# Kernel optimization log

Hardware: AMD Instinct MI355X
Metric: run time of the kernel (lower is better)

Reference implementation:

```python
import jax, jax.numpy as jnp
import numpy as np

N = [40000, 10000, 2500, 625, 157]  # vertex counts per mesh level (0 = full res)
K = 6


def _propagate(x, row, col, norm, n):
    # x: [B, N_in, C]; gather neighbor feats, weight by norm, scatter-add to rows
    msg = x[:, col, :] * norm[None, :, None]          # [B, E, C]
    return jnp.zeros((x.shape[0], n, x.shape[2]), x.dtype).at[:, row, :].add(msg)


def cheb_conv(x, edge_index, W, b, n):
    # Chebyshev graph conv with sym-normalized adjacency (lambda_max=2 / CoMA convention)
    row, col = edge_index[0], edge_index[1]
    deg = jnp.zeros((n,), x.dtype).at[row].add(jnp.ones(row.shape, x.dtype))
    dinv = jnp.where(deg > 0, deg ** -0.5, jnp.zeros_like(deg))
    norm = dinv[row] * dinv[col]
    Tx0 = x
    out = jnp.einsum('bnc,cd->bnd', Tx0, W[0])
    Tx1 = _propagate(Tx0, row, col, norm, n)
    out = out + jnp.einsum('bnc,cd->bnd', Tx1, W[1])
    for k in range(2, W.shape[0]):
        Tx2 = 2.0 * _propagate(Tx1, row, col, norm, n) - Tx0
        out = out + jnp.einsum('bnc,cd->bnd', Tx2, W[k])
        Tx0, Tx1 = Tx1, Tx2
    return out + b


def pool(x, row, col, val, n_out):
    # sparse COO upsampling: out[:, row] += val * x[:, col]  (Pool() in torch source)
    msg = x[:, col, :] * val[None, :, None]
    return jnp.zeros((x.shape[0], n_out, x.shape[2]), x.dtype).at[:, row, :].add(msg)


def setup_inputs() -> dict:
    key = jax.random.key(0)
    ks = iter(jax.random.split(key, 64))
    B, latent = 16, 128
    inp = {}
    inp['x'] = jax.random.normal(next(ks), (B, latent), jnp.float32)
    inp['lin_w'] = jax.random.normal(next(ks), (latent, N[4] * 64), jnp.float32) * 0.05
    inp['lin_b'] = jnp.zeros((N[4] * 64,), jnp.float32)
    for i in range(4):
        inp[f'edge{i}'] = jax.random.randint(next(ks), (2, 6 * N[i]), 0, N[i])
    for i in range(4):
        nnz = 3 * N[i]
        inp[f'up{i}_row'] = jax.random.randint(next(ks), (nnz,), 0, N[i])
        inp[f'up{i}_col'] = jax.random.randint(next(ks), (nnz,), 0, N[i + 1])
        inp[f'up{i}_val'] = jax.random.uniform(next(ks), (nnz,), jnp.float32)
    # Deblock Cheb weights: (in,out) = (64,64),(64,32),(32,32),(32,32); final (32,3)
    for j, (ci, co) in enumerate([(64, 64), (64, 32), (32, 32), (32, 32)], start=1):
        inp[f'W{j}'] = jax.random.normal(next(ks), (K, ci, co), jnp.float32) * 0.05
        inp[f'b{j}'] = jnp.zeros((co,), jnp.float32)
    inp['Wout'] = jax.random.normal(next(ks), (K, 32, 3), jnp.float32) * 0.05
    inp['bout'] = jnp.zeros((3,), jnp.float32)
    return inp


def reference(x, lin_w, lin_b, edge0, edge1, edge2, edge3,
              up0_row, up0_col, up0_val, up1_row, up1_col, up1_val,
              up2_row, up2_col, up2_val, up3_row, up3_col, up3_val,
              W1, b1, W2, b2, W3, b3, W4, b4, Wout, bout):
    B = x.shape[0]
    h = (x @ lin_w + lin_b).reshape(B, N[4], 64)        # latent -> coarsest mesh
    edges = [edge0, edge1, edge2, edge3]
    ups = [(up0_row, up0_col, up0_val), (up1_row, up1_col, up1_val),
           (up2_row, up2_col, up2_val), (up3_row, up3_col, up3_val)]
    Ws = [(W1, b1), (W2, b2), (W3, b3), (W4, b4)]
    for j in range(4):
        lvl = 3 - j  # deblock j upsamples to mesh level lvl (coarse -> fine)
        row, col, val = ups[lvl]
        h = pool(h, row, col, val, N[lvl])
        h = jax.nn.elu(cheb_conv(h, edges[lvl], Ws[j][0], Ws[j][1], N[lvl]))
    return cheb_conv(h, edge0, Wout, bout, N[0])        # [B, 40000, 3]
```

## Files before the change

### kernel.cpp

```cpp
#include <hip/hip_runtime.h>
#include <math.h>

#define TB 256
#define SCAN_TOT 106250
#define SCAN_NB  104

typedef __bf16 bf16x8 __attribute__((ext_vector_type(8)));
typedef float f32x4 __attribute__((ext_vector_type(4)));
typedef float f32x2 __attribute__((ext_vector_type(2)));

static __device__ __forceinline__ int gtid() { return blockIdx.x * blockDim.x + threadIdx.x; }

static __device__ __forceinline__ void fma4(float4& a, float s, const float4 b) {
  a.x = fmaf(s, b.x, a.x); a.y = fmaf(s, b.y, a.y);
  a.z = fmaf(s, b.z, a.z); a.w = fmaf(s, b.w, a.w);
}

static __device__ __forceinline__ float bfus(unsigned short u) {
  union { unsigned u; float f; } c; c.u = ((unsigned)u) << 16; return c.f;
}
static __device__ __forceinline__ unsigned pk2(float a, float b) {
  union { unsigned u; __bf16 h[2]; } c;
  c.h[0] = (__bf16)a; c.h[1] = (__bf16)b;
  return c.u;
}
static __device__ __forceinline__ unsigned short us1(float a) {
  union { unsigned short u; __bf16 h; } c; c.h = (__bf16)a; return c.u;
}
static __device__ __forceinline__ f32x2 unpk(unsigned u) {
  union { unsigned u; float f; } lo, hi;
  lo.u = u << 16; hi.u = u & 0xffff0000u;
  f32x2 r; r.x = lo.f; r.y = hi.f; return r;
}

__global__ void fill_kernel(float* __restrict__ p, int n, float v) {
  int i = gtid(); if (i < n) p[i] = v;
}

__global__ void zero_int_kernel(int* __restrict__ p, int n) {
  int i = gtid(); if (i < n) p[i] = 0;
}

struct SegD {
  const int* rows[8];
  const int* cols[8];
  const float* vals[8];
  int start[8];
  int degb[8];
};

__global__ void count_all_kernel(SegD sg, int total, int* __restrict__ deg) {
  int t = gtid(); if (t >= total) return;
  int seg = 0;
  #pragma unroll
  for (int q = 1; q < 8; ++q) seg += (t >= sg.start[q]);
  int i = t - sg.start[seg];
  atomicAdd(&deg[sg.degb[seg] + sg.rows[seg][i]], 1);
}

__global__ void fill_all_kernel(SegD sg, int total, const int* __restrict__ deg,
                                const int* __restrict__ offs, int* __restrict__ cursor,
                                int2* __restrict__ cwc) {
  int t = gtid(); if (t >= total) return;
  int seg = 0;
  #pragma unroll
  for (int q = 1; q < 8; ++q) seg += (t >= sg.start[q]);
  int i = t - sg.start[seg];
  int db = sg.degb[seg];
  int r = sg.rows[seg][i];
  int c = sg.cols[seg][i];
  int p = atomicAdd(&cursor[db + r], 1);
  int idx = offs[db + r] + p;
  float w;
  if (sg.vals[seg]) {
    w = sg.vals[seg][i];
  } else {
    int dc = deg[db + c];
    w = rsqrtf((float)deg[db + r]) * (dc > 0 ? rsqrtf((float)dc) : 0.f);
  }
  int2 o; o.x = c; o.y = __float_as_int(w);
  cwc[idx] = o;
}

__global__ void scan_phase1(const int* __restrict__ in, int* __restrict__ bsum) {
  __shared__ int wsum[4];
  int blk = blockIdx.x, t = threadIdx.x;
  int base = blk * 1024 + t * 4;
  int s = 0;
  #pragma unroll
  for (int q = 0; q < 4; ++q) { int i = base + q; if (i < SCAN_TOT) s += in[i]; }
  #pragma unroll
  for (int o = 32; o > 0; o >>= 1) s += __shfl_xor(s, o, 64);
  int lane = t & 63, wid = t >> 6;
  if (lane == 0) wsum[wid] = s;
  __syncthreads();
  if (t == 0) bsum[blk] = wsum[0] + wsum[1] + wsum[2] + wsum[3];
}

__global__ void scan_phase2(int* __restrict__ bsum, int* __restrict__ offs_end) {
  int t = threadIdx.x;
  int v = (t < SCAN_NB) ? bsum[t] : 0;
  int lane = t & 63, wid = t >> 6;
  int p = v;
  #pragma unroll
  for (int o = 1; o < 64; o <<= 1) { int u = __shfl_up(p, o, 64); if (lane >= o) p += u; }
  __shared__ int w0tot;
  if (wid == 0 && lane == 63) w0tot = p;
  __syncthreads();
  int incl = p + (wid ? w0tot : 0);
  if (t < SCAN_NB) bsum[t] = incl - v;
  if (t == 127) offs_end[0] = incl;
}

__global__ void scan_phase3(const int* __restrict__ in, const int* __restrict__ bbase,
                            int* __restrict__ offs, int* __restrict__ cursor) {
  __shared__ int wsum[4];
  int blk = blockIdx.x, t = threadIdx.x;
  int base = blk * 1024 + t * 4;
  int v[4]; int s = 0;
  #pragma unroll
  for (int q = 0; q < 4; ++q) { int i = base + q; v[q] = (i < SCAN_TOT) ? in[i] : 0; s += v[q]; }
  int lane = t & 63, wid = t >> 6;
  int p = s;
  #pragma unroll
  for (int o = 1; o < 64; o <<= 1) { int u = __shfl_up(p, o, 64); if (lane >= o) p += u; }
  if (lane == 63) wsum[wid] = p;
  __syncthreads();
  int woff = 0;
  #pragma unroll
  for (int q = 0; q < 4; ++q) woff += (q < wid) ? wsum[q] : 0;
  int ex = bbase[blk] + woff + p - s;
  #pragma unroll
  for (int q = 0; q < 4; ++q) {
    int i = base + q;
    if (i < SCAN_TOT) { offs[i] = ex; cursor[i] = 0; ex += v[q]; }
  }
}

__global__ void wconv_kernel(const float* __restrict__ W, unsigned* __restrict__ Wt) {
  int p = gtid();
  if (p >= 6 * 32 * 16) return;
  int kk2 = p & 15;
  int col = (p >> 4) & 31;
  int kidx = p >> 9;
  float v0 = W[kidx * 1024 + (2 * kk2) * 32 + col];
  float v1 = W[kidx * 1024 + (2 * kk2 + 1) * 32 + col];
  Wt[(kidx * 32 + col) * 16 + kk2] = pk2(v0, v1);
}

__global__ void pool_kernel(const float4* __restrict__ x, const int* __restrict__ offs,
                            const int2* __restrict__ cwc,
                            float4* __restrict__ out, int n, int xs4, int xoff4,
                            int os4, int osh) {
  int t = gtid();
  if (t >= n * os4) return;
  int v = t >> osh, j = t & (os4 - 1);
  int s = offs[v], e = offs[v + 1];
  float4 a = {0.f, 0.f, 0.f, 0.f};
  for (int i = s; i < e; ++i) {
    int2 cw = cwc[i];
    fma4(a, __int_as_float(cw.y), x[(long long)cw.x * xs4 + xoff4 + j]);
  }
  out[t] = a;
}

template<int SRC>
__global__ void __launch_bounds__(256)
pool_mfma_kernel(const void* __restrict__ xsrc, const int* __restrict__ offs,
                 const int2* __restrict__ cwc,
                 uint4* __restrict__ Xout, uint4* __restrict__ b5out,
                 const uint4* __restrict__ Wtk5, int n) {
  int lane = threadIdx.x & 63;
  int v = (blockIdx.x << 2) | (threadIdx.x >> 6);
  if (v >= n) return;
  int g = lane >> 4, c15 = lane & 15;
  int s = offs[v], e = offs[v + 1];
  int deg = e - s;
  float a[8];
  #pragma unroll
  for (int q = 0; q < 8; ++q) a[q] = 0.f;

  if (deg > 0) {
    if (SRC == 0) {
      const float4* x = (const float4*)xsrc;
      float4 x0[4], x1[4]; float ww[4];
      #pragma unroll
      for (int p = 0; p < 4; ++p) {
        int idx = s + (p < deg ? p : 0);
        int2 cw = cwc[idx];
        ww[p] = (p < deg) ? __int_as_float(cw.y) : 0.f;
        const float4* xr = x + (long long)cw.x * 128 + c15 * 8 + g * 2;
        x0[p] = xr[0]; x1[p] = xr[1];
      }
      #pragma unroll
      for (int p = 0; p < 4; ++p) {
        float w = ww[p];
        a[0] = fmaf(w, x0[p].x, a[0]); a[1] = fmaf(w, x0[p].y, a[1]);
        a[2] = fmaf(w, x0[p].z, a[2]); a[3] = fmaf(w, x0[p].w, a[3]);
        a[4] = fmaf(w, x1[p].x, a[4]); a[5] = fmaf(w, x1[p].y, a[5]);
        a[6] = fmaf(w, x1[p].z, a[6]); a[7] = fmaf(w, x1[p].w, a[7]);
      }
      for (int i = s + 4; i < e; ++i) {
        int2 cw = cwc[i];
        float w = __int_as_float(cw.y);
        const float4* xr = x + (long long)cw.x * 128 + c15 * 8 + g * 2;
        float4 y0 = xr[0], y1 = xr[1];
        a[0] = fmaf(w, y0.x, a[0]); a[1] = fmaf(w, y0.y, a[1]);
        a[2] = fmaf(w, y0.z, a[2]); a[3] = fmaf(w, y0.w, a[3]);
        a[4] = fmaf(w, y1.x, a[4]); a[5] = fmaf(w, y1.y, a[5]);
        a[6] = fmaf(w, y1.z, a[6]); a[7] = fmaf(w, y1.w, a[7]);
      }
    } else {
      const uint4* x = (const uint4*)xsrc;
      uint4 bv[4]; float ww[4];
      #pragma unroll
      for (int p = 0; p < 4; ++p) {
        int idx = s + (p < deg ? p : 0);
        int2 cw = cwc[idx];
        ww[p] = (p < deg) ? __int_as_float(cw.y) : 0.f;
        bv[p] = x[(long long)cw.x * 64 + c15 * 4 + g];
      }
      #pragma unroll
      for (int p = 0; p < 4; ++p) {
        f32x2 w2 = {ww[p], ww[p]};
        f32x2 r0 = __builtin_elementwise_fma(w2, unpk(bv[p].x), f32x2{a[0], a[1]});
        f32x2 r1 = __builtin_elementwise_fma(w2, unpk(bv[p].y), f32x2{a[2], a[3]});
        f32x2 r2 = __builtin_elementwise_fma(w2, unpk(bv[p].z), f32x2{a[4], a[5]});
        f32x2 r3 = __builtin_elementwise_fma(w2, unpk(bv[p].w), f32x2{a[6], a[7]});
        a[0] = r0.x; a[1] = r0.y; a[2] = r1.x; a[3] = r1.y;
        a[4] = r2.x; a[5] = r2.y; a[6] = r3.x; a[7] = r3.y;
      }
      for (int i = s + 4; i < e; ++i) {
        int2 cw = cwc[i];
        float w = __int_as_float(cw.y);
        f32x2 w2 = {w, w};
        uint4 xv = x[(long long)cw.x * 64 + c15 * 4 + g];
        f32x2 r0 = __builtin_elementwise_fma(w2, unpk(xv.x), f32x2{a[0], a[1]});
        f32x2 r1 = __builtin_elementwise_fma(w2, unpk(xv.y), f32x2{a[2], a[3]});
        f32x2 r2 = __builtin_elementwise_fma(w2, unpk(xv.z), f32x2{a[4], a[5]});
        f32x2 r3 = __builtin_elementwise_fma(w2, unpk(xv.w), f32x2{a[6], a[7]});
        a[0] = r0.x; a[1] = r0.y; a[2] = r1.x; a[3] = r1.y;
        a[4] = r2.x; a[5] = r2.y; a[6] = r3.x; a[7] = r3.y;
      }
    }
  }
  union { uint4 u; bf16x8 b; } Au;
  Au.u.x = pk2(a[0], a[1]); Au.u.y = pk2(a[2], a[3]);
  Au.u.z = pk2(a[4], a[5]); Au.u.w = pk2(a[6], a[7]);
  Xout[(long long)v * 64 + c15 * 4 + g] = Au.u;

  union { uint4 u; bf16x8 b; } B0u, B1u;
  B0u.u = Wtk5[c15 * 4 + g];
  B1u.u = Wtk5[(16 + c15) * 4 + g];
  f32x4 z = {0.f, 0.f, 0.f, 0.f};
  f32x4 m0 = __builtin_amdgcn_mfma_f32_16x16x32_bf16(Au.b, B0u.b, z, 0, 0, 0);
  f32x4 m1 = __builtin_amdgcn_mfma_f32_16x16x32_bf16(Au.b, B1u.b, z, 0, 0, 0);
  uint4 o;
  o.x = pk2(m0[0], m1[0]); o.y = pk2(m0[1], m1[1]);
  o.z = pk2(m0[2], m1[2]); o.w = pk2(m0[3], m1[3]);
  b5out[(long long)v * 64 + g * 16 + c15] = o;
}

template<int CIN, int COUT>
__global__ void cheb_step_kernel(const float* __restrict__ X,
                                 const float* __restrict__ b1,
                                 float* __restrict__ b2o,
                                 const float* __restrict__ Wk,
                                 const float* __restrict__ bias,
                                 const int* __restrict__ offs,
                                 const int2* __restrict__ cwc,
                                 int n, int LB, int mode) {
  constexpr int CS = COUT / 8;
  constexpr int LCS = (CS == 8) ? 3 : 2;
  constexpr int W4 = COUT / 4;
  __shared__ float sW[CIN * COUT];
  for (int i = threadIdx.x; i < CIN * COUT; i += blockDim.x) sW[i] = Wk[i];
  __syncthreads();
  int t = gtid();
  int BI = 1 << LB;
  if (t >= n * BI * CS) return;
  int cs = t & (CS - 1);
  int r = t >> LCS;
  int v = r >> LB;
  int bi = r & (BI - 1);
  float4 a0 = {0.f, 0.f, 0.f, 0.f}, a1 = {0.f, 0.f, 0.f, 0.f};
  const float4* Xr = (const float4*)(X + (long long)r * CIN);
  const float4* wbase = ((const float4*)sW) + cs * 2;
  #pragma unroll
  for (int c4 = 0; c4 < CIN / 4; ++c4) {
    float4 xv = Xr[c4];
    const float4* w = wbase + (c4 * 4) * W4;
    fma4(a0, xv.x, w[0]); fma4(a1, xv.x, w[1]); w += W4;
    fma4(a0, xv.y, w[0]); fma4(a1, xv.y, w[1]); w += W4;
    fma4(a0, xv.z, w[0]); fma4(a1, xv.z, w[1]); w += W4;
    fma4(a0, xv.w, w[0]); fma4(a1, xv.w, w[1]);
  }
  if (mode >= 1) {
    float sc = (mode == 3) ? 1.f : 2.f;
    int s = offs[v], e = offs[v + 1];
    const float4* b14 = (const float4*)b1;
    for (int i = s; i < e; ++i) {
      int2 cw = cwc[i];
      float w = __int_as_float(cw.y) * sc;
      long long rb = (long long)((cw.x << LB) | bi) * W4 + cs * 2;
      fma4(a0, w, b14[rb]); fma4(a1, w, b14[rb + 1]);
    }
  }
  float4* Or = ((float4*)b2o) + (long long)r * W4 + cs * 2;
  if (mode >= 2) {
    float4 p0 = Or[0], p1 = Or[1];
    a0.x -= p0.x; a0.y -= p0.y; a0.z -= p0.z; a0.w -= p0.w;
    a1.x -= p1.x; a1.y -= p1.y; a1.z -= p1.z; a1.w -= p1.w;
  }
  if (mode == 3) {
    const float* bs = bias + cs * 8;
    a0.x += bs[0]; a0.y += bs[1]; a0.z += bs[2]; a0.w += bs[3];
    a1.x += bs[4]; a1.y += bs[5]; a1.z += bs[6]; a1.w += bs[7];
    a0.x = a0.x > 0.f ? a0.x : expm1f(a0.x);
    a0.y = a0.y > 0.f ? a0.y : expm1f(a0.y);
    a0.z = a0.z > 0.f ? a0.z : expm1f(a0.z);
    a0.w = a0.w > 0.f ? a0.w : expm1f(a0.w);
    a1.x = a1.x > 0.f ? a1.x : expm1f(a1.x);
    a1.y = a1.y > 0.f ? a1.y : expm1f(a1.y);
    a1.z = a1.z > 0.f ? a1.z : expm1f(a1.z);
    a1.w = a1.w > 0.f ? a1.w : expm1f(a1.w);
  }
  Or[0] = a0; Or[1] = a1;
}

__global__ void __launch_bounds__(256)
cheb_mfma32_kernel(const uint4* __restrict__ X,
                   const uint4* __restrict__ b1,
                   uint4* __restrict__ b2o,
                   const uint4* __restrict__ Wtk,
                   const float* __restrict__ bias,
                   const int* __restrict__ offs,
                   const int2* __restrict__ cwc,
                   int n, int mode) {
  int lane = threadIdx.x & 63;
  int v = (blockIdx.x << 2) | (threadIdx.x >> 6);
  if (v >= n) return;
  int g = lane >> 4;
  int c15 = lane & 15;

  union { uint4 u; bf16x8 b; } Au, B0u, B1u;
  Au.u = X[(long long)v * 64 + c15 * 4 + g];
  B0u.u = Wtk[c15 * 4 + g];
  B1u.u = Wtk[(16 + c15) * 4 + g];

  f32x4 z = {0.f, 0.f, 0.f, 0.f};
  f32x4 m0 = __builtin_amdgcn_mfma_f32_16x16x32_bf16(Au.b, B0u.b, z, 0, 0, 0);
  f32x4 m1 = __builtin_amdgcn_mfma_f32_16x16x32_bf16(Au.b, B1u.b, z, 0, 0, 0);
  f32x2 acc[4];
  #pragma unroll
  for (int q = 0; q < 4; ++q) { acc[q].x = m0[q]; acc[q].y = m1[q]; }

  long long own = (long long)v * 64 + g * 16 + c15;
  if (mode >= 1) {
    float sc = (mode == 3) ? 1.f : 2.f;
    int s = offs[v], e = offs[v + 1];
    int deg = e - s;
    if (deg > 0) {
      uint4 bv[8]; float ww[8];
      #pragma unroll
      for (int p = 0; p < 8; ++p) {
        int idx = s + (p < deg ? p : 0);
        int2 cw = cwc[idx];
        ww[p] = (p < deg) ? __int_as_float(cw.y) * sc : 0.f;
        bv[p] = b1[(long long)cw.x * 64 + g * 16 + c15];
      }
      #pragma unroll
      for (int p = 0; p < 8; ++p) {
        f32x2 w2 = {ww[p], ww[p]};
        acc[0] = __builtin_elementwise_fma(w2, unpk(bv[p].x), acc[0]);
        acc[1] = __builtin_elementwise_fma(w2, unpk(bv[p].y), acc[1]);
        acc[2] = __builtin_elementwise_fma(w2, unpk(bv[p].z), acc[2]);
        acc[3] = __builtin_elementwise_fma(w2, unpk(bv[p].w), acc[3]);
      }
      for (int i = s + 8; i < e; ++i) {
        int2 cw = cwc[i];
        float w = __int_as_float(cw.y) * sc;
        f32x2 w2 = {w, w};
        uint4 xv = b1[(long long)cw.x * 64 + g * 16 + c15];
        acc[0] = __builtin_elementwise_fma(w2, unpk(xv.x), acc[0]);
        acc[1] = __builtin_elementwise_fma(w2, unpk(xv.y), acc[1]);
        acc[2] = __builtin_elementwise_fma(w2, unpk(xv.z), acc[2]);
        acc[3] = __builtin_elementwise_fma(w2, unpk(xv.w), acc[3]);
      }
    }
  }
  if (mode >= 2) {
    uint4 pv = b2o[own];
    acc[0] -= unpk(pv.x); acc[1] -= unpk(pv.y);
    acc[2] -= unpk(pv.z); acc[3] -= unpk(pv.w);
  }
  if (mode == 3) {
    float bs0 = bias[c15], bs1 = bias[16 + c15];
    unsigned short* o = (unsigned short*)b2o;
    long long lb = ((long long)v * 16 + 4 * g) * 32;
    #pragma unroll
    for (int q = 0; q < 4; ++q) {
      float a = acc[q].x + bs0;
      float b = acc[q].y + bs1;
      a = a > 0.f ? a : expm1f(a);
      b = b > 0.f ? b : expm1f(b);
      o[lb + q * 32 + c15] = us1(a);
      o[lb + q * 32 + 16 + c15] = us1(b);
    }
  } else {
    uint4 o;
    o.x = pk2(acc[0].x, acc[0].y); o.y = pk2(acc[1].x, acc[1].y);
    o.z = pk2(acc[2].x, acc[2].y); o.w = pk2(acc[3].x, acc[3].y);
    b2o[own] = o;
  }
}

__global__ void gemm_out_all_kernel(const uint4* __restrict__ X, const float* __restrict__ W,
                                    unsigned short* __restrict__ c_all, int nr) {
  __shared__ float sW[576];
  for (int i = threadIdx.x; i < 576; i += blockDim.x) sW[i] = W[i];
  __syncthreads();
  int r = gtid();
  if (r >= nr) return;
  const uint4* Xr = X + (long long)r * 4;
  float xa[32];
  #pragma unroll
  for (int q = 0; q < 4; ++q) {
    uint4 xv = Xr[q];
    f32x2 p0 = unpk(xv.x), p1 = unpk(xv.y), p2 = unpk(xv.z), p3 = unpk(xv.w);
    xa[q * 8 + 0] = p0.x; xa[q * 8 + 1] = p0.y;
    xa[q * 8 + 2] = p1.x; xa[q * 8 + 3] = p1.y;
    xa[q * 8 + 4] = p2.x; xa[q * 8 + 5] = p2.y;
    xa[q * 8 + 6] = p3.x; xa[q * 8 + 7] = p3.y;
  }
  float acc[18];
  #pragma unroll
  for (int i = 0; i < 18; ++i) acc[i] = 0.f;
  #pragma unroll
  for (int c = 0; c < 32; ++c) {
    float xc = xa[c];
    #pragma unroll
    for (int k = 0; k < 6; ++k) {
      acc[k * 3 + 0] = fmaf(xc, sW[k * 96 + c * 3 + 0], acc[k * 3 + 0]);
      acc[k * 3 + 1] = fmaf(xc, sW[k * 96 + c * 3 + 1], acc[k * 3 + 1]);
      acc[k * 3 + 2] = fmaf(xc, sW[k * 96 + c * 3 + 2], acc[k * 3 + 2]);
    }
  }
  #pragma unroll
  for (int k = 0; k < 6; ++k) {
    unsigned short* o = c_all + ((long long)k * nr + r) * 3;
    o[0] = us1(acc[k * 3 + 0]);
    o[1] = us1(acc[k * 3 + 1]);
    o[2] = us1(acc[k * 3 + 2]);
  }
}

__global__ void cheb_out_step_kernel(const unsigned short* __restrict__ c_all, int k,
                                     const float* __restrict__ b1,
                                     float* __restrict__ b2o,
                                     const float* __restrict__ bias,
                                     const int* __restrict__ offs,
                                     const int2* __restrict__ cwc,
                                     int n, float* __restrict__ dout, int mode) {
  int r = gtid();
  if (r >= n * 16) return;
  int v = r >> 4, bi = r & 15;
  const unsigned short* cr = c_all + ((long long)k * n * 16 + r) * 3;
  float a0 = bfus(cr[0]), a1 = bfus(cr[1]), a2 = bfus(cr[2]);
  if (mode >= 1) {
    float sc = (mode == 3) ? 1.f : 2.f;
    int s = offs[v], e = offs[v + 1];
    for (int i = s; i < e; ++i) {
      int2 cw = cwc[i];
      float w = __int_as_float(cw.y) * sc;
      const float* br = b1 + (long long)((cw.x << 4) | bi) * 3;
      a0 = fmaf(w, br[0], a0); a1 = fmaf(w, br[1], a1); a2 = fmaf(w, br[2], a2);
    }
  }
  if (mode >= 2) {
    const float* p = b2o + (long long)r * 3;
    a0 -= p[0]; a1 -= p[1]; a2 -= p[2];
  }
  if (mode == 3) {
    a0 += bias[0]; a1 += bias[1]; a2 += bias[2];
    float* o = dout + ((long long)bi * n + v) * 3;
    o[0] = a0; o[1] = a1; o[2] = a2;
  } else {
    float* o = b2o + (long long)r * 3;
    o[0] = a0; o[1] = a1; o[2] = a2;
  }
}

__global__ void linear_kernel(const float* __restrict__ x, const float* __restrict__ w,
                              const float* __restrict__ bias, float* __restrict__ out) {
  int t = gtid();
  const int TOT = 157 * 16 * 64;
  if (t >= TOT) return;
  int c = t & 63;
  int b = (t >> 6) & 15;
  int v = t >> 10;
  int colw = v * 64 + c;
  float acc = bias[colw];
  const float* xr = x + b * 128;
  for (int k = 0; k < 128; ++k) acc = fmaf(xr[k], w[k * 10048 + colw], acc);
  out[t] = acc;
}

extern "C" void kernel_launch(void* const* d_in, const int* in_sizes, int n_in,
                              void* d_out, int out_size, void* d_ws, size_t ws_size,
                              hipStream_t stream) {
  const int N[4] = {40000, 10000, 2500, 625};
  const int E[4] = {240000, 60000, 15000, 3750};
  const int NNZ[4] = {120000, 30000, 7500, 1875};
  const int DP[4] = {0, 40000, 50000, 52500};
  const int DE[4] = {53125, 93125, 103125, 105625};
  const int ITEMS = 478125;

  const float* x     = (const float*)d_in[0];
  const float* lin_w = (const float*)d_in[1];
  const float* lin_b = (const float*)d_in[2];
  const int* edge[4] = {(const int*)d_in[3], (const int*)d_in[4], (const int*)d_in[5], (const int*)d_in[6]};
  const int* up_row[4]; const int* up_col[4]; const float* up_val[4];
  for (int i = 0; i < 4; ++i) {
    up_row[i] = (const int*)d_in[7 + 3 * i];
    up_col[i] = (const int*)d_in[8 + 3 * i];
    up_val[i] = (const float*)d_in[9 + 3 * i];
  }
  const float* W_[5] = {(const float*)d_in[19], (const float*)d_in[21], (const float*)d_in[23],
                        (const float*)d_in[25], (const float*)d_in[27]};
  const float* b_[5] = {(const float*)d_in[20], (const float*)d_in[22], (const float*)d_in[24],
                        (const float*)d_in[26], (const float*)d_in[28]};

  char* ws = (char*)d_ws;
  size_t off = 0;
  auto alloc = [&](size_t bytes) -> void* {
    void* p = ws + off;
    off = (off + bytes + 255) & ~(size_t)255;
    return p;
  };
  auto cdiv = [](int a, int b) { return (a + b - 1) / b; };

  float* slot[4];
  for (int i = 0; i < 4; ++i) slot[i] = (float*)alloc(20480000ull);
  uint4* Ab = (uint4*)alloc(40960000ull);
  uint4* Bb = (uint4*)alloc(40960000ull);
  uint4* Cb = (uint4*)alloc(40960000ull);
  unsigned short* c_all = (unsigned short*)alloc((size_t)6 * 640000 * 3 * 2);
  float* ob1 = (float*)alloc((size_t)640000 * 3 * 4);
  float* ob2 = (float*)alloc((size_t)640000 * 3 * 4);
  int* deg_all    = (int*)alloc(SCAN_TOT * 4);
  int* cursor_all = (int*)alloc(SCAN_TOT * 4);
  int* offs_all   = (int*)alloc((SCAN_TOT + 1) * 4);
  int* bsum       = (int*)alloc(SCAN_NB * 4);
  int2* cwc_arena = (int2*)alloc((size_t)ITEMS * 8);
  uint4* Wt2 = (uint4*)alloc(6 * 128 * 16);
  uint4* Wt3 = (uint4*)alloc(6 * 128 * 16);

  if (off > ws_size) {
    fill_kernel<<<cdiv(out_size, TB), TB, 0, stream>>>((float*)d_out, out_size,
                                                       (float)(ws_size >> 20));
    return;
  }

  SegD sg;
  int cum = 0;
  for (int l = 0; l < 4; ++l) {
    sg.rows[l] = up_row[l]; sg.cols[l] = up_col[l]; sg.vals[l] = up_val[l];
    sg.start[l] = cum; sg.degb[l] = DP[l]; cum += NNZ[l];
  }
  for (int l = 0; l < 4; ++l) {
    sg.rows[4 + l] = edge[l]; sg.cols[4 + l] = edge[l] + E[l]; sg.vals[4 + l] = nullptr;
    sg.start[4 + l] = cum; sg.degb[4 + l] = DE[l]; cum += E[l];
  }
  zero_int_kernel<<<cdiv(SCAN_TOT, TB), TB, 0, stream>>>(deg_all, SCAN_TOT);
  count_all_kernel<<<cdiv(ITEMS, TB), TB, 0, stream>>>(sg, ITEMS, deg_all);
  scan_phase1<<<SCAN_NB, TB, 0, stream>>>(deg_all, bsum);
  scan_phase2<<<1, 128, 0, stream>>>(bsum, offs_all + SCAN_TOT);
  scan_phase3<<<SCAN_NB, TB, 0, stream>>>(deg_all, bsum, offs_all, cursor_all);
  fill_all_kernel<<<cdiv(ITEMS, TB), TB, 0, stream>>>(sg, ITEMS, deg_all, offs_all,
                                                      cursor_all, cwc_arena);
  wconv_kernel<<<cdiv(3072, TB), TB, 0, stream>>>(W_[2], (unsigned*)Wt2);
  wconv_kernel<<<cdiv(3072, TB), TB, 0, stream>>>(W_[3], (unsigned*)Wt3);

  linear_kernel<<<cdiv(157 * 16 * 64, TB), TB, 0, stream>>>(x, lin_w, lin_b, slot[0]);
  float* H = slot[0];
  float* A = slot[1];
  float* B = slot[2];
  float* C = slot[3];

  const int CINA[2]  = {64, 64};
  const int COUTA[2] = {64, 32};

  for (int j = 0; j < 2; ++j) {
    int lvl = 3 - j;
    int n = N[lvl];
    int cin = CINA[j], cout = COUTA[j];
    int os4 = 16 * cin / 4;
    int osh = (os4 == 256) ? 8 : 7;
    const int* offs_p = offs_all + DP[lvl];
    const int* offs_e = offs_all + DE[lvl];

    pool_kernel<<<cdiv(n * os4, TB), TB, 0, stream>>>(
        (const float4*)H, offs_p, cwc_arena, (float4*)A, n, os4, 0, os4, osh);

    int cs = cout / 8;
    dim3 g(cdiv(n * 16 * cs, TB));
    auto step = [&](const float* b1, float* b2o, int k, int mode) {
      const float* Wk = W_[j] + (size_t)k * cin * cout;
      if (cin == 64 && cout == 64)
        hipLaunchKernelGGL((cheb_step_kernel<64, 64>), g, dim3(TB), 0, stream,
                           A, b1, b2o, Wk, b_[j], offs_e, cwc_arena, n, 4, mode);
      else
        hipLaunchKernelGGL((cheb_step_kernel<64, 32>), g, dim3(TB), 0, stream,
                           A, b1, b2o, Wk, b_[j], offs_e, cwc_arena, n, 4, mode);
    };
    step(nullptr, B, 5, 0);
    step(B, C, 4, 1);
    step(C, B, 3, 2);
    step(B, C, 2, 2);
    step(C, B, 1, 2);
    step(B, C, 0, 3);

    float* tmp = H; H = C; C = tmp;
  }
  float* freeA = A;
  float* freeB = B;
  float* freeC = C;

  uint4* Ab1 = (uint4*)freeA;
  uint4* Bb1 = (uint4*)freeB;
  uint4* Cb1 = (uint4*)freeC;
  {
    int n = N[1];
    dim3 gmf(n / 4);
    hipLaunchKernelGGL((pool_mfma_kernel<0>), gmf, dim3(256), 0, stream,
                       (const void*)H, offs_all + DP[1], cwc_arena,
                       Ab1, Bb1, Wt2 + (size_t)5 * 128, n);
    auto dstep = [&](const uint4* b1, uint4* b2o, int k, int mode) {
      cheb_mfma32_kernel<<<gmf, dim3(256), 0, stream>>>(
          Ab1, b1, b2o, Wt2 + (size_t)k * 128, b_[2],
          offs_all + DE[1], cwc_arena, n, mode);
    };
    dstep(Bb1, Cb1, 4, 1);
    dstep(Cb1, Bb1, 3, 2);
    dstep(Bb1, Cb1, 2, 2);
    dstep(Cb1, Bb1, 1, 2);
    dstep(Bb1, Cb1, 0, 3);
  }

  {
    int n = N[0];
    int nr = n * 16;
    const int* offs_e = offs_all + DE[0];
    dim3 gmf(n / 4);

    hipLaunchKernelGGL((pool_mfma_kernel<1>), gmf, dim3(256), 0, stream,
                       (const void*)Cb1, offs_all + DP[0], cwc_arena,
                       Ab, Bb, Wt3 + (size_t)5 * 128, n);

    auto dstep = [&](const uint4* b1, uint4* b2o, int k, int mode) {
      cheb_mfma32_kernel<<<gmf, dim3(256), 0, stream>>>(
          Ab, b1, b2o, Wt3 + (size_t)k * 128, b_[3],
          offs_e, cwc_arena, n, mode);
    };
    dstep(Bb, Cb, 4, 1);
    dstep(Cb, Bb, 3, 2);
    dstep(Bb, Cb, 2, 2);
    dstep(Cb, Bb, 1, 2);
    dstep(Bb, Cb, 0, 3);

    dim3 gr(cdiv(nr, TB));
    gemm_out_all_kernel<<<gr, dim3(TB), 0, stream>>>((const uint4*)Cb, W_[4], c_all, nr);
    float* dout = (float*)d_out;
    auto ostep = [&](const float* b1, float* b2o, int k, int mode) {
      cheb_out_step_kernel<<<gr, dim3(TB), 0, stream>>>(
          c_all, k, b1, b2o, b_[4], offs_e, cwc_arena, n, dout, mode);
    };
    ostep(nullptr, ob1, 5, 0);
    ostep(ob1, ob2, 4, 1);
    ostep(ob2, ob1, 3, 2);
    ostep(ob1, ob2, 2, 2);
    ostep(ob2, ob1, 1, 2);
    ostep(ob1, ob2, 0, 3);
  }
}
```

Baseline: 748.9 us.

## Split finest-level decoder into two batch halves to shrink working buffers

Processes the level-0 pool, Chebyshev steps and output conv in two passes of 8 batch samples each. The pool and cheb MFMA kernels are templated on rows-per-vertex R so that one 16-row MFMA tile covers two vertices when R is 8. Intermediate buffers are halved, so each pass's working set is smaller and more of it may stay in the MI355X's large last-level cache. The trade-off is twice as many kernel launches, re-reading the edge lists per pass, and more complex index mapping.

```diff
diff --git a/kernel.cpp b/kernel.cpp
--- a/kernel.cpp
+++ b/kernel.cpp
@@ -164,17 +164,22 @@
   out[t] = a;
 }
 
-template<int SRC>
+template<int SRC, int R>
 __global__ void __launch_bounds__(256)
 pool_mfma_kernel(const void* __restrict__ xsrc, const int* __restrict__ offs,
                  const int2* __restrict__ cwc,
                  uint4* __restrict__ Xout, uint4* __restrict__ b5out,
-                 const uint4* __restrict__ Wtk5, int n) {
+                 const uint4* __restrict__ Wtk5, int browoff, int n) {
+  constexpr int VW = 16 / R;
+  constexpr int U4V = 4 * R;
   int lane = threadIdx.x & 63;
-  int v = (blockIdx.x << 2) | (threadIdx.x >> 6);
-  if (v >= n) return;
+  int vbase = ((blockIdx.x << 2) | (threadIdx.x >> 6)) * VW;
+  if (vbase >= n) return;
   int g = lane >> 4, c15 = lane & 15;
-  int s = offs[v], e = offs[v + 1];
+  int va = vbase + c15 / R;
+  int ra = c15 % R;
+  int srow = browoff + ra;
+  int s = offs[va], e = offs[va + 1];
   int deg = e - s;
   float a[8];
   #pragma unroll
@@ -189,7 +194,7 @@
         int idx = s + (p < deg ? p : 0);
         int2 cw = cwc[idx];
         ww[p] = (p < deg) ? __int_as_float(cw.y) : 0.f;
-        const float4* xr = x + (long long)cw.x * 128 + c15 * 8 + g * 2;
+        const float4* xr = x + (long long)cw.x * 128 + srow * 8 + g * 2;
         x0[p] = xr[0]; x1[p] = xr[1];
       }
       #pragma unroll
@@ -203,7 +208,7 @@
       for (int i = s + 4; i < e; ++i) {
         int2 cw = cwc[i];
         float w = __int_as_float(cw.y);
-        const float4* xr = x + (long long)cw.x * 128 + c15 * 8 + g * 2;
+        const float4* xr = x + (long long)cw.x * 128 + srow * 8 + g * 2;
         float4 y0 = xr[0], y1 = xr[1];
         a[0] = fmaf(w, y0.x, a[0]); a[1] = fmaf(w, y0.y, a[1]);
         a[2] = fmaf(w, y0.z, a[2]); a[3] = fmaf(w, y0.w, a[3]);
@@ -218,7 +223,7 @@
         int idx = s + (p < deg ? p : 0);
         int2 cw = cwc[idx];
         ww[p] = (p < deg) ? __int_as_float(cw.y) : 0.f;
-        bv[p] = x[(long long)cw.x * 64 + c15 * 4 + g];
+        bv[p] = x[(long long)cw.x * 64 + srow * 4 + g];
       }
       #pragma unroll
       for (int p = 0; p < 4; ++p) {
@@ -234,7 +239,7 @@
         int2 cw = cwc[i];
         float w = __int_as_float(cw.y);
         f32x2 w2 = {w, w};
-        uint4 xv = x[(long long)cw.x * 64 + c15 * 4 + g];
+        uint4 xv = x[(long long)cw.x * 64 + srow * 4 + g];
         f32x2 r0 = __builtin_elementwise_fma(w2, unpk(xv.x), f32x2{a[0], a[1]});
         f32x2 r1 = __builtin_elementwise_fma(w2, unpk(xv.y), f32x2{a[2], a[3]});
         f32x2 r2 = __builtin_elementwise_fma(w2, unpk(xv.z), f32x2{a[4], a[5]});
@@ -247,7 +252,7 @@
   union { uint4 u; bf16x8 b; } Au;
   Au.u.x = pk2(a[0], a[1]); Au.u.y = pk2(a[2], a[3]);
   Au.u.z = pk2(a[4], a[5]); Au.u.w = pk2(a[6], a[7]);
-  Xout[(long long)v * 64 + c15 * 4 + g] = Au.u;
+  Xout[(long long)va * U4V + ra * 4 + g] = Au.u;
 
   union { uint4 u; bf16x8 b; } B0u, B1u;
   B0u.u = Wtk5[c15 * 4 + g];
@@ -255,10 +260,12 @@
   f32x4 z = {0.f, 0.f, 0.f, 0.f};
   f32x4 m0 = __builtin_amdgcn_mfma_f32_16x16x32_bf16(Au.b, B0u.b, z, 0, 0, 0);
   f32x4 m1 = __builtin_amdgcn_mfma_f32_16x16x32_bf16(Au.b, B1u.b, z, 0, 0, 0);
+  int vl = vbase + (4 * g) / R;
+  int gl = g % (R / 4);
   uint4 o;
   o.x = pk2(m0[0], m1[0]); o.y = pk2(m0[1], m1[1]);
   o.z = pk2(m0[2], m1[2]); o.w = pk2(m0[3], m1[3]);
-  b5out[(long long)v * 64 + g * 16 + c15] = o;
+  b5out[(long long)vl * U4V + gl * 16 + c15] = o;
 }
 
 template<int CIN, int COUT>
@@ -328,6 +335,7 @@
   Or[0] = a0; Or[1] = a1;
 }
 
+template<int R>
 __global__ void __launch_bounds__(256)
 cheb_mfma32_kernel(const uint4* __restrict__ X,
                    const uint4* __restrict__ b1,
@@ -337,14 +345,18 @@
                    const int* __restrict__ offs,
                    const int2* __restrict__ cwc,
                    int n, int mode) {
+  constexpr int VW = 16 / R;
+  constexpr int U4V = 4 * R;
   int lane = threadIdx.x & 63;
-  int v = (blockIdx.x << 2) | (threadIdx.x >> 6);
-  if (v >= n) return;
+  int vbase = ((blockIdx.x << 2) | (threadIdx.x >> 6)) * VW;
+  if (vbase >= n) return;
   int g = lane >> 4;
   int c15 = lane & 15;
+  int va = vbase + c15 / R;
+  int ra = c15 % R;
 
   union { uint4 u; bf16x8 b; } Au, B0u, B1u;
-  Au.u = X[(long long)v * 64 + c15 * 4 + g];
+  Au.u = X[(long long)va * U4V + ra * 4 + g];
   B0u.u = Wtk[c15 * 4 + g];
   B1u.u = Wtk[(16 + c15) * 4 + g];
 
@@ -355,10 +367,12 @@
   #pragma unroll
   for (int q = 0; q < 4; ++q) { acc[q].x = m0[q]; acc[q].y = m1[q]; }
 
-  long long own = (long long)v * 64 + g * 16 + c15;
+  int vl = vbase + (4 * g) / R;
+  int gl = g % (R / 4);
+  long long own = (long long)vl * U4V + gl * 16 + c15;
   if (mode >= 1) {
     float sc = (mode == 3) ? 1.f : 2.f;
-    int s = offs[v], e = offs[v + 1];
+    int s = offs[vl], e = offs[vl + 1];
     int deg = e - s;
     if (deg > 0) {
       uint4 bv[8]; float ww[8];
@@ -367,7 +381,7 @@
         int idx = s + (p < deg ? p : 0);
         int2 cw = cwc[idx];
         ww[p] = (p < deg) ? __int_as_float(cw.y) * sc : 0.f;
-        bv[p] = b1[(long long)cw.x * 64 + g * 16 + c15];
+        bv[p] = b1[(long long)cw.x * U4V + gl * 16 + c15];
       }
       #pragma unroll
       for (int p = 0; p < 8; ++p) {
@@ -381,7 +395,7 @@
         int2 cw = cwc[i];
         float w = __int_as_float(cw.y) * sc;
         f32x2 w2 = {w, w};
-        uint4 xv = b1[(long long)cw.x * 64 + g * 16 + c15];
+        uint4 xv = b1[(long long)cw.x * U4V + gl * 16 + c15];
         acc[0] = __builtin_elementwise_fma(w2, unpk(xv.x), acc[0]);
         acc[1] = __builtin_elementwise_fma(w2, unpk(xv.y), acc[1]);
         acc[2] = __builtin_elementwise_fma(w2, unpk(xv.z), acc[2]);
@@ -397,7 +411,7 @@
   if (mode == 3) {
     float bs0 = bias[c15], bs1 = bias[16 + c15];
     unsigned short* o = (unsigned short*)b2o;
-    long long lb = ((long long)v * 16 + 4 * g) * 32;
+    long long lb = ((long long)vl * R + gl * 4) * 32;
     #pragma unroll
     for (int q = 0; q < 4; ++q) {
       float a = acc[q].x + bs0;
@@ -461,11 +475,14 @@
                                      const float* __restrict__ bias,
                                      const int* __restrict__ offs,
                                      const int2* __restrict__ cwc,
-                                     int n, float* __restrict__ dout, int mode) {
+                                     int n, int lb, int boff,
+                                     float* __restrict__ dout, int mode) {
+  int BI = 1 << lb;
   int r = gtid();
-  if (r >= n * 16) return;
-  int v = r >> 4, bi = r & 15;
-  const unsigned short* cr = c_all + ((long long)k * n * 16 + r) * 3;
+  if (r >= n * BI) return;
+  int v = r >> lb, bi = r & (BI - 1);
+  int nr = n << lb;
+  const unsigned short* cr = c_all + ((long long)k * nr + r) * 3;
   float a0 = bfus(cr[0]), a1 = bfus(cr[1]), a2 = bfus(cr[2]);
   if (mode >= 1) {
     float sc = (mode == 3) ? 1.f : 2.f;
@@ -473,7 +490,7 @@
     for (int i = s; i < e; ++i) {
       int2 cw = cwc[i];
       float w = __int_as_float(cw.y) * sc;
-      const float* br = b1 + (long long)((cw.x << 4) | bi) * 3;
+      const float* br = b1 + (long long)((cw.x << lb) | bi) * 3;
       a0 = fmaf(w, br[0], a0); a1 = fmaf(w, br[1], a1); a2 = fmaf(w, br[2], a2);
     }
   }
@@ -483,7 +500,7 @@
   }
   if (mode == 3) {
     a0 += bias[0]; a1 += bias[1]; a2 += bias[2];
-    float* o = dout + ((long long)bi * n + v) * 3;
+    float* o = dout + ((long long)(boff + bi) * n + v) * 3;
     o[0] = a0; o[1] = a1; o[2] = a2;
   } else {
     float* o = b2o + (long long)r * 3;
@@ -542,12 +559,12 @@
 
   float* slot[4];
   for (int i = 0; i < 4; ++i) slot[i] = (float*)alloc(20480000ull);
-  uint4* Ab = (uint4*)alloc(40960000ull);
-  uint4* Bb = (uint4*)alloc(40960000ull);
-  uint4* Cb = (uint4*)alloc(40960000ull);
-  unsigned short* c_all = (unsigned short*)alloc((size_t)6 * 640000 * 3 * 2);
-  float* ob1 = (float*)alloc((size_t)640000 * 3 * 4);
-  float* ob2 = (float*)alloc((size_t)640000 * 3 * 4);
+  uint4* Ab = (uint4*)alloc(20480000ull);
+  uint4* Bb = (uint4*)alloc(20480000ull);
+  uint4* Cb = (uint4*)alloc(20480000ull);
+  unsigned short* c_all = (unsigned short*)alloc((size_t)6 * 320000 * 3 * 2);
+  float* ob1 = (float*)alloc((size_t)320000 * 3 * 4);
+  float* ob2 = (float*)alloc((size_t)320000 * 3 * 4);
   int* deg_all    = (int*)alloc(SCAN_TOT * 4);
   int* cursor_all = (int*)alloc(SCAN_TOT * 4);
   int* offs_all   = (int*)alloc((SCAN_TOT + 1) * 4);
@@ -623,23 +640,20 @@
 
     float* tmp = H; H = C; C = tmp;
   }
-  float* freeA = A;
-  float* freeB = B;
-  float* freeC = C;
-
-  uint4* Ab1 = (uint4*)freeA;
-  uint4* Bb1 = (uint4*)freeB;
-  uint4* Cb1 = (uint4*)freeC;
+
+  uint4* Ab1 = (uint4*)A;
+  uint4* Bb1 = (uint4*)B;
+  uint4* Cb1 = (uint4*)C;
   {
     int n = N[1];
     dim3 gmf(n / 4);
-    hipLaunchKernelGGL((pool_mfma_kernel<0>), gmf, dim3(256), 0, stream,
+    hipLaunchKernelGGL((pool_mfma_kernel<0, 16>), gmf, dim3(256), 0, stream,
                        (const void*)H, offs_all + DP[1], cwc_arena,
-                       Ab1, Bb1, Wt2 + (size_t)5 * 128, n);
+                       Ab1, Bb1, Wt2 + (size_t)5 * 128, 0, n);
     auto dstep = [&](const uint4* b1, uint4* b2o, int k, int mode) {
-      cheb_mfma32_kernel<<<gmf, dim3(256), 0, stream>>>(
-          Ab1, b1, b2o, Wt2 + (size_t)k * 128, b_[2],
-          offs_all + DE[1], cwc_arena, n, mode);
+      hipLaunchKernelGGL((cheb_mfma32_kernel<16>), gmf, dim3(256), 0, stream,
+                         Ab1, b1, b2o, Wt2 + (size_t)k * 128, b_[2],
+                         offs_all + DE[1], cwc_arena, n, mode);
     };
     dstep(Bb1, Cb1, 4, 1);
     dstep(Cb1, Bb1, 3, 2);
@@ -650,37 +664,39 @@
 
   {
     int n = N[0];
-    int nr = n * 16;
+    int nr = n * 8;
+    const int* offs_p = offs_all + DP[0];
     const int* offs_e = offs_all + DE[0];
-    dim3 gmf(n / 4);
-
-    hipLaunchKernelGGL((pool_mfma_kernel<1>), gmf, dim3(256), 0, stream,
-                       (const void*)Cb1, offs_all + DP[0], cwc_arena,
-                       Ab, Bb, Wt3 + (size_t)5 * 128, n);
-
-    auto dstep = [&](const uint4* b1, uint4* b2o, int k, int mode) {
-      cheb_mfma32_kernel<<<gmf, dim3(256), 0, stream>>>(
-          Ab, b1, b2o, Wt3 + (size_t)k * 128, b_[3],
-          offs_e, cwc_arena, n, mode);
-    };
-    dstep(Bb, Cb, 4, 1);
-    dstep(Cb, Bb, 3, 2);
-    dstep(Bb, Cb, 2, 2);
-    dstep(Cb, Bb, 1, 2);
-    dstep(Bb, Cb, 0, 3);
-
+    dim3 gmf(n / 8);
     dim3 gr(cdiv(nr, TB));
-    gemm_out_all_kernel<<<gr, dim3(TB), 0, stream>>>((const uint4*)Cb, W_[4], c_all, nr);
     float* dout = (float*)d_out;
-    auto ostep = [&](const float* b1, float* b2o, int k, int mode) {
-      cheb_out_step_kernel<<<gr, dim3(TB), 0, stream>>>(
-          c_all, k, b1, b2o, b_[4], offs_e, cwc_arena, n, dout, mode);
-    };
-    ostep(nullptr, ob1, 5, 0);
-    ostep(ob1, ob2, 4, 1);
-    ostep(ob2, ob1, 3, 2);
-    ostep(ob1, ob2, 2, 2);
-    ostep(ob2, ob1, 1, 2);
-    ostep(ob1, ob2, 0, 3);
-  }
-}
+
+    for (int bg = 0; bg < 2; ++bg) {
+      hipLaunchKernelGGL((pool_mfma_kernel<1, 8>), gmf, dim3(256), 0, stream,
+                         (const void*)Cb1, offs_p, cwc_arena,
+                         Ab, Bb, Wt3 + (size_t)5 * 128, bg * 8, n);
+      auto dstep = [&](const uint4* b1, uint4* b2o, int k, int mode) {
+        hipLaunchKernelGGL((cheb_mfma32_kernel<8>), gmf, dim3(256), 0, stream,
+                           Ab, b1, b2o, Wt3 + (size_t)k * 128, b_[3],
+                           offs_e, cwc_arena, n, mode);
+      };
+      dstep(Bb, Cb, 4, 1);
+      dstep(Cb, Bb, 3, 2);
+      dstep(Bb, Cb, 2, 2);
+      dstep(Cb, Bb, 1, 2);
+      dstep(Bb, Cb, 0, 3);
+
+      gemm_out_all_kernel<<<gr, dim3(TB), 0, stream>>>((const uint4*)Cb, W_[4], c_all, nr);
+      auto ostep = [&](const float* b1, float* b2o, int k, int mode) {
+        cheb_out_step_kernel<<<gr, dim3(TB), 0, stream>>>(
+            c_all, k, b1, b2o, b_[4], offs_e, cwc_arena, n, 3, bg * 8, dout, mode);
+      };
+      ostep(nullptr, ob1, 5, 0);
+      ostep(ob1, ob2, 4, 1);
+      ostep(ob2, ob1, 3, 2);
+      ostep(ob1, ob2, 2, 2);
+      ostep(ob2, ob1, 1, 2);
+      ostep(ob1, ob2, 0, 3);
+    }
+  }
+}
```

After: 826.5 us. 1.1x slower.
